# Performance work log

Hardware: AMD Instinct MI355X
Metric: run time of the kernel (lower is better)

## Reference

```python
import jax, jax.numpy as jnp
import numpy as np

WS = 8      # window size
SS = 4      # shift size
NH = 4      # num heads
EPS = 1e-5
MLP_RATIO = 4


def _win_part(x, ws):
    # x: [B,D,H,W,C] -> [B*nD*nH*nW, ws^3, C]
    B, D, H, W, C = x.shape
    x = x.reshape(B, D // ws, ws, H // ws, ws, W // ws, ws, C)
    x = x.transpose(0, 1, 3, 5, 2, 4, 6, 7)
    return x.reshape(-1, ws * ws * ws, C)


def _win_rev(w, ws, B, D, H, W):
    C = w.shape[-1]
    x = w.reshape(B, D // ws, H // ws, W // ws, ws, ws, ws, C)
    x = x.transpose(0, 1, 4, 2, 5, 3, 6, 7)
    return x.reshape(B, D, H, W, C)


def _ln(x, g, b):
    m = jnp.mean(x, axis=-1, keepdims=True)
    v = jnp.mean((x - m) ** 2, axis=-1, keepdims=True)
    return (x - m) / jnp.sqrt(v + EPS) * g + b


def _rel_index(ws):
    coords = np.stack(np.meshgrid(np.arange(ws), np.arange(ws), np.arange(ws), indexing='ij'))  # [3,ws,ws,ws]
    cf = coords.reshape(3, -1)                      # [3, ws^3]
    rel = (cf[:, :, None] - cf[:, None, :]).transpose(1, 2, 0) + (ws - 1)  # [N,N,3]
    return rel[..., 0] * (2 * ws - 1) ** 2 + rel[..., 1] * (2 * ws - 1) + rel[..., 2]


def _attn_mask(D, H, W, ws, ss):
    img = np.zeros((1, D, H, W, 1), dtype=np.float32)
    cnt = 0
    sl = (slice(0, -ws), slice(-ws, -ss), slice(-ss, None))
    for d in sl:
        for h in sl:
            for w in sl:
                img[:, d, h, w, :] = cnt
                cnt += 1
    mw = np.asarray(_win_part(jnp.asarray(img), ws))[..., 0]  # [nW, ws^3]
    diff = mw[:, None, :] - mw[:, :, None]
    return np.where(diff != 0, -100.0, 0.0).astype(np.float32)


def setup_inputs() -> dict:
    key = jax.random.key(0)
    ks = jax.random.split(key, 12)
    B, D, H, W, C = 1, 16, 64, 64, 128
    mh = MLP_RATIO * C
    s = 0.02
    return {
        'x': jax.random.normal(ks[0], (B, D, H, W, C), jnp.float32),
        'attn_mask': jnp.asarray(_attn_mask(D, H, W, WS, SS)),
        'rel_index': jnp.asarray(_rel_index(WS), jnp.int32),
        'rel_bias': jax.random.normal(ks[1], ((2 * WS - 1) ** 3, NH), jnp.float32) * s,
        'qkv_w': jax.random.normal(ks[2], (3 * C, C), jnp.float32) * s,
        'qkv_b': jnp.zeros((3 * C,), jnp.float32),
        'proj_w': jax.random.normal(ks[3], (C, C), jnp.float32) * s,
        'proj_b': jnp.zeros((C,), jnp.float32),
        'norm1_g': jnp.ones((C,), jnp.float32),
        'norm1_b': jnp.zeros((C,), jnp.float32),
        'norm2_g': jnp.ones((C,), jnp.float32),
        'norm2_b': jnp.zeros((C,), jnp.float32),
        'mlp_w1': jax.random.normal(ks[4], (mh, C), jnp.float32) * s,
        'mlp_b1': jnp.zeros((mh,), jnp.float32),
        'mlp_w2': jax.random.normal(ks[5], (C, mh), jnp.float32) * s,
        'mlp_b2': jnp.zeros((C,), jnp.float32),
    }


def reference(x, attn_mask, rel_index, rel_bias, qkv_w, qkv_b, proj_w, proj_b,
              norm1_g, norm1_b, norm2_g, norm2_b, mlp_w1, mlp_b1, mlp_w2, mlp_b2):
    B, D, H, W, C = x.shape
    ws, ss, nh = WS, SS, NH
    hd = C // nh
    scale = hd ** -0.5
    N = ws ** 3
    shortcut = x
    h = _ln(x, norm1_g, norm1_b)
    h = jnp.roll(h, (-ss, -ss, -ss), axis=(1, 2, 3))
    xw = _win_part(h, ws)                 # [B_, N, C]
    B_ = xw.shape[0]
    nW = attn_mask.shape[0]
    qkv = xw @ qkv_w.T + qkv_b            # [B_, N, 3C]
    qkv = qkv.reshape(B_, N, 3, nh, hd).transpose(2, 0, 3, 1, 4)  # [3,B_,h,N,hd]
    q, k, v = qkv[0] * scale, qkv[1], qkv[2]
    attn = jnp.einsum('bhnd,bhmd->bhnm', q, k)
    rpe = rel_bias[rel_index.reshape(-1)].reshape(N, N, nh).transpose(2, 0, 1)  # [h,N,N]
    attn = attn + rpe[None]
    attn = attn.reshape(B_ // nW, nW, nh, N, N) + attn_mask[None, :, None]
    attn = jax.nn.softmax(attn.reshape(B_, nh, N, N), axis=-1)
    out = jnp.einsum('bhnm,bhmd->bhnd', attn, v).transpose(0, 2, 1, 3).reshape(B_, N, C)
    out = out @ proj_w.T + proj_b
    out = _win_rev(out, ws, B, D, H, W)
    out = jnp.roll(out, (ss, ss, ss), axis=(1, 2, 3))
    x = shortcut + out
    h2 = _ln(x, norm2_g, norm2_b)
    h2 = jax.nn.gelu(h2 @ mlp_w1.T + mlp_b1, approximate=False)
    return x + h2 @ mlp_w2.T + mlp_b2
```

## Files before the change

### kernel.cpp

```cpp
#include <hip/hip_runtime.h>
#include <math.h>

typedef __bf16 bf16;
typedef __bf16 bf16x8 __attribute__((ext_vector_type(8)));
typedef float f32x4 __attribute__((ext_vector_type(4)));
typedef unsigned short u16;
typedef u16 u16x2 __attribute__((ext_vector_type(2)));
typedef u16 u16x4 __attribute__((ext_vector_type(4)));

__device__ __forceinline__ float b2f(u16 b) {
  return (float)__builtin_bit_cast(bf16, b);
}

__global__ void sniff_k(const unsigned* __restrict__ xw_, int* __restrict__ flag) {
  if (threadIdx.x == 0 && blockIdx.x == 0) {
    int cnt = 0;
    for (int i = 0; i < 256; i++) {
      unsigned e = (xw_[i] >> 7) & 0xFFu;
      cnt += (e >= 100u && e <= 140u) ? 1 : 0;
    }
    *flag = (cnt >= 150) ? 1 : 0;
  }
}

__global__ __launch_bounds__(256) void canon_big_k(const void* __restrict__ src,
                                                   bf16* __restrict__ dst,
                                                   const int* __restrict__ flag) {
  int i = (blockIdx.x * 256 + threadIdx.x) * 8;
  if (*flag) {
    *(bf16x8*)&dst[i] = *(const bf16x8*)((const bf16*)src + i);
  } else {
    const float* s = (const float*)src + i;
    bf16x8 v;
#pragma unroll
    for (int j = 0; j < 8; j++) v[j] = (bf16)s[j];
    *(bf16x8*)&dst[i] = v;
  }
}

struct CanonArgs {
  const void* src[13];
  bf16* dst[13];
  int n[13];
};

__global__ __launch_bounds__(256) void canon_small_k(CanonArgs a,
                                                     const int* __restrict__ flag) {
  int ti = blockIdx.y;
  int i = blockIdx.x * 256 + threadIdx.x;
  if (i >= a.n[ti]) return;
  if (*flag)
    a.dst[ti][i] = ((const bf16*)a.src[ti])[i];
  else
    a.dst[ti][i] = (bf16)((const float*)a.src[ti])[i];
}

__global__ __launch_bounds__(256) void rpe_k(const int* __restrict__ ridx,
                                             const bf16* __restrict__ rbias,
                                             bf16* __restrict__ rpeT) {
  int t = blockIdx.x * 256 + threadIdx.x;
  int q = t & 511, m = (t >> 9) & 511, h = t >> 18;
  rpeT[t] = rbias[ridx[q * 512 + m] * 4 + h];
}

template <int ROLL>
__global__ __launch_bounds__(256) void ln_k(const bf16* __restrict__ x,
                                            const bf16* __restrict__ g,
                                            const bf16* __restrict__ bsh,
                                            bf16* __restrict__ out) {
  int wave = threadIdx.x >> 6, lane = threadIdx.x & 63;
  int tok = blockIdx.x * 4 + wave;
  size_t src;
  if (ROLL) {
    int win = tok >> 9, pos = tok & 511;
    int rd = (win >> 6) * 8 + (pos >> 6);
    int rh = ((win >> 3) & 7) * 8 + ((pos >> 3) & 7);
    int rw = (win & 7) * 8 + (pos & 7);
    int od = (rd + 4) & 15, oh = (rh + 4) & 63, ow = (rw + 4) & 63;
    src = (size_t)((od * 64 + oh) * 64 + ow) * 128;
  } else {
    src = (size_t)tok * 128;
  }
  int ch = lane * 2;
  u16x2 xv = *(const u16x2*)(x + src + ch);
  float f0 = b2f(xv[0]), f1 = b2f(xv[1]);
  float s = f0 + f1, sq = f0 * f0 + f1 * f1;
#pragma unroll
  for (int d = 1; d < 64; d <<= 1) {
    s += __shfl_xor(s, d);
    sq += __shfl_xor(sq, d);
  }
  float mean = s * (1.f / 128.f);
  float var = sq * (1.f / 128.f) - mean * mean;
  float rstd = rsqrtf(fmaxf(var, 0.f) + 1e-5f);
  u16x2 gv = *(const u16x2*)(g + ch), bv = *(const u16x2*)(bsh + ch);
  u16x2 ov;
  ov[0] = __builtin_bit_cast(u16, (bf16)((f0 - mean) * rstd * b2f(gv[0]) + b2f(bv[0])));
  ov[1] = __builtin_bit_cast(u16, (bf16)((f1 - mean) * rstd * b2f(gv[1]) + b2f(bv[1])));
  *(u16x2*)(out + (size_t)tok * 128 + ch) = ov;
}

template <int EPI, int N_, int K_>
__global__ __launch_bounds__(256) void gemm_k(const bf16* __restrict__ A,
                                              const bf16* __restrict__ B,
                                              const bf16* __restrict__ bias,
                                              void* __restrict__ outv,
                                              const bf16* __restrict__ resid,
                                              const int* __restrict__ flag) {
  __shared__ __align__(16) u16 As[128 * 72];
  __shared__ __align__(16) u16 Bs[128 * 72];
  const int t = threadIdx.x;
  const int wave = t >> 6, lane = t & 63, l15 = lane & 15, quad = lane >> 4;
  const int m0 = blockIdx.x * 128, n0 = blockIdx.y * 128;
  int fl = 0;
  if constexpr (EPI == 3) fl = *flag;
  f32x4 acc[4][4] = {};
  const int wr = (wave >> 1) * 64, wc = (wave & 1) * 64;
  const int srow = t >> 3, scol = (t & 7) * 8;
  for (int kc = 0; kc < K_; kc += 64) {
    bf16x8 av[4], bv[4];
#pragma unroll
    for (int p = 0; p < 4; p++) {
      int row = p * 32 + srow;
      av[p] = *(const bf16x8*)(A + (size_t)(m0 + row) * K_ + kc + scol);
      bv[p] = *(const bf16x8*)(B + (size_t)(n0 + row) * K_ + kc + scol);
    }
    __syncthreads();
#pragma unroll
    for (int p = 0; p < 4; p++) {
      int row = p * 32 + srow;
      *(bf16x8*)&As[row * 72 + scol] = av[p];
      *(bf16x8*)&Bs[row * 72 + scol] = bv[p];
    }
    __syncthreads();
#pragma unroll
    for (int ks = 0; ks < 2; ks++) {
      bf16x8 a[4], b[4];
#pragma unroll
      for (int i = 0; i < 4; i++) {
        a[i] = *(const bf16x8*)&As[(wr + i * 16 + l15) * 72 + ks * 32 + quad * 8];
        b[i] = *(const bf16x8*)&Bs[(wc + i * 16 + l15) * 72 + ks * 32 + quad * 8];
      }
#pragma unroll
      for (int i = 0; i < 4; i++)
#pragma unroll
        for (int j = 0; j < 4; j++)
          acc[i][j] =
              __builtin_amdgcn_mfma_f32_16x16x32_bf16(a[i], b[j], acc[i][j], 0, 0, 0);
    }
  }
  const float qscale = 0.17677669529663687f;
#pragma unroll
  for (int i = 0; i < 4; i++) {
#pragma unroll
    for (int r = 0; r < 4; r++) {
      int tok = m0 + wr + i * 16 + quad * 4 + r;
      size_t obase = 0;
      if constexpr (EPI == 1) {
        int win = tok >> 9, pos = tok & 511;
        int rd = (win >> 6) * 8 + (pos >> 6);
        int rh = ((win >> 3) & 7) * 8 + ((pos >> 3) & 7);
        int rw = (win & 7) * 8 + (pos & 7);
        int od = (rd + 4) & 15, oh = (rh + 4) & 63, ow = (rw + 4) & 63;
        obase = (size_t)((od * 64 + oh) * 64 + ow) * 128;
      } else if constexpr (EPI != 0) {
        obase = (size_t)tok * N_;
      }
#pragma unroll
      for (int j = 0; j < 4; j++) {
        int gn = n0 + wc + j * 16 + l15;
        float v = acc[i][j][r] + (float)bias[gn];
        if constexpr (EPI == 0) {
          int tensor = gn >> 7, c = gn & 127, head = c >> 5, d = c & 31;
          if (tensor == 0) v *= qscale;
          int win = tok >> 9, pos = tok & 511;
          size_t off = ((((size_t)tensor * 4 + head) * 128 + win) * 512 + pos) * 32 + d;
          ((bf16*)outv)[off] = (bf16)v;
        } else if constexpr (EPI == 1) {
          v += (float)resid[obase + gn];
          ((bf16*)outv)[obase + gn] = (bf16)v;
        } else if constexpr (EPI == 2) {
          v = 0.5f * v * (1.f + erff(v * 0.70710678118654752f));
          ((bf16*)outv)[obase + gn] = (bf16)v;
        } else {
          v += (float)resid[obase + gn];
          if (fl)
            ((bf16*)outv)[obase + gn] = (bf16)v;
          else
            ((float*)outv)[obase + gn] = v;
        }
      }
    }
  }
}

__global__ __launch_bounds__(256) void attn_k(const bf16* __restrict__ qkv,
                                              const bf16* __restrict__ rpeT,
                                              bf16* __restrict__ att) {
  __shared__ __align__(16) u16 sVt[32 * 72];
  __shared__ __align__(16) u16 sP[4][32 * 72];
  __shared__ __align__(16) u16 sR[64 * 136];
  __shared__ unsigned char lbl[512];
  const int t = threadIdx.x;
  const int p = blockIdx.x;
  const int win = ((p >> 7) << 3) | (p & 7);
  const int j = (p >> 3) & 15;
  const int head = j >> 2, qc = j & 3;
  const int wave = t >> 6, lane = t & 63, l15 = lane & 15, quad = lane >> 4;

  {
    int wd = win >> 6, wh = (win >> 3) & 7, wwi = win & 7;
    for (int pp = t; pp < 512; pp += 256) {
      int gd = wd * 8 + (pp >> 6), gh = wh * 8 + ((pp >> 3) & 7),
          gw = wwi * 8 + (pp & 7);
      int ld = gd < 8 ? 0 : (gd < 12 ? 1 : 2);
      int lh = gh < 56 ? 0 : (gh < 60 ? 1 : 2);
      int lw = gw < 56 ? 0 : (gw < 60 ? 1 : 2);
      lbl[pp] = (unsigned char)((ld << 4) | (lh << 2) | lw);
    }
  }
  __syncthreads();

  const size_t hw32 = (size_t)512 * 32;
  const bf16* qp = qkv + ((size_t)(0 * 4 + head) * 128 + win) * hw32;
  const bf16* kp = qkv + ((size_t)(1 * 4 + head) * 128 + win) * hw32;
  const bf16* vp = qkv + ((size_t)(2 * 4 + head) * 128 + win) * hw32;
  const int qbase = qc * 128 + wave * 32;

  int lq[2][4];
#pragma unroll
  for (int mt = 0; mt < 2; mt++)
#pragma unroll
    for (int r = 0; r < 4; r++) lq[mt][r] = lbl[qbase + mt * 16 + quad * 4 + r];

  bf16x8 qa[2];
#pragma unroll
  for (int mt = 0; mt < 2; mt++)
    qa[mt] = *(const bf16x8*)(qp + (size_t)(qbase + mt * 16 + l15) * 32 + quad * 8);

  f32x4 O[2][2] = {};
  float ms[2][4], ls[2][4];
#pragma unroll
  for (int mt = 0; mt < 2; mt++)
#pragma unroll
    for (int r = 0; r < 4; r++) {
      ms[mt][r] = -1e30f;
      ls[mt][r] = 0.f;
    }
  const f32x4 zf = {0.f, 0.f, 0.f, 0.f};
  const bf16* rpeh = rpeT + (size_t)head * 512 * 512;

  for (int kt = 0; kt < 8; kt++) {
    __syncthreads();
    {
      int row = t >> 2, c4 = t & 3;
      bf16x8 vv = *(const bf16x8*)(vp + (size_t)(kt * 64 + row) * 32 + c4 * 8);
#pragma unroll
      for (int jj = 0; jj < 8; jj++)
        sVt[(c4 * 8 + jj) * 72 + row] = __builtin_bit_cast(u16, vv[jj]);
    }
    {
      int rr = t >> 4, cc = (t & 15) * 8;
#pragma unroll
      for (int pp = 0; pp < 4; pp++) {
        int row = pp * 16 + rr;
        bf16x8 rv = *(const bf16x8*)(rpeh + (size_t)(kt * 64 + row) * 512 +
                                     qc * 128 + cc);
        *(bf16x8*)&sR[row * 136 + cc] = rv;
      }
    }
    __syncthreads();

    f32x4 S[2][4];
#pragma unroll
    for (int nt = 0; nt < 4; nt++) {
      bf16x8 kb =
          *(const bf16x8*)(kp + (size_t)(kt * 64 + nt * 16 + l15) * 32 + quad * 8);
      S[0][nt] = __builtin_amdgcn_mfma_f32_16x16x32_bf16(qa[0], kb, zf, 0, 0, 0);
      S[1][nt] = __builtin_amdgcn_mfma_f32_16x16x32_bf16(qa[1], kb, zf, 0, 0, 0);
    }
#pragma unroll
    for (int nt = 0; nt < 4; nt++) {
      int lk = lbl[kt * 64 + nt * 16 + l15];
#pragma unroll
      for (int mt = 0; mt < 2; mt++) {
        u16x4 rv = *(const u16x4*)&sR[(nt * 16 + l15) * 136 + mt * 16 + quad * 4];
#pragma unroll
        for (int r = 0; r < 4; r++) {
          float bv = b2f(rv[r]);
          if (lq[mt][r] != lk) bv -= 100.f;
          S[mt][nt][r] += bv;
        }
      }
    }
#pragma unroll
    for (int mt = 0; mt < 2; mt++)
#pragma unroll
      for (int r = 0; r < 4; r++) {
        float mx = fmaxf(fmaxf(S[mt][0][r], S[mt][1][r]),
                         fmaxf(S[mt][2][r], S[mt][3][r]));
        mx = fmaxf(mx, __shfl_xor(mx, 1));
        mx = fmaxf(mx, __shfl_xor(mx, 2));
        mx = fmaxf(mx, __shfl_xor(mx, 4));
        mx = fmaxf(mx, __shfl_xor(mx, 8));
        float mnew = fmaxf(ms[mt][r], mx);
        float alpha = __expf(fminf(ms[mt][r] - mnew, 0.f));
        ms[mt][r] = mnew;
        float rs = 0.f;
#pragma unroll
        for (int nt = 0; nt < 4; nt++) {
          float pe = __expf(fminf(S[mt][nt][r] - mnew, 0.f));
          S[mt][nt][r] = pe;
          rs += pe;
        }
        rs += __shfl_xor(rs, 1);
        rs += __shfl_xor(rs, 2);
        rs += __shfl_xor(rs, 4);
        rs += __shfl_xor(rs, 8);
        ls[mt][r] = ls[mt][r] * alpha + rs;
        O[mt][0][r] *= alpha;
        O[mt][1][r] *= alpha;
      }
    u16* pw = sP[wave];
#pragma unroll
    for (int mt = 0; mt < 2; mt++)
#pragma unroll
      for (int nt = 0; nt < 4; nt++)
#pragma unroll
        for (int r = 0; r < 4; r++)
          pw[(mt * 16 + quad * 4 + r) * 72 + nt * 16 + l15] =
              __builtin_bit_cast(u16, (bf16)S[mt][nt][r]);
    __syncthreads();
#pragma unroll
    for (int s = 0; s < 2; s++) {
      bf16x8 pa0 = *(const bf16x8*)&pw[l15 * 72 + s * 32 + quad * 8];
      bf16x8 pa1 = *(const bf16x8*)&pw[(16 + l15) * 72 + s * 32 + quad * 8];
      bf16x8 vb0 = *(const bf16x8*)&sVt[l15 * 72 + s * 32 + quad * 8];
      bf16x8 vb1 = *(const bf16x8*)&sVt[(16 + l15) * 72 + s * 32 + quad * 8];
      O[0][0] = __builtin_amdgcn_mfma_f32_16x16x32_bf16(pa0, vb0, O[0][0], 0, 0, 0);
      O[0][1] = __builtin_amdgcn_mfma_f32_16x16x32_bf16(pa0, vb1, O[0][1], 0, 0, 0);
      O[1][0] = __builtin_amdgcn_mfma_f32_16x16x32_bf16(pa1, vb0, O[1][0], 0, 0, 0);
      O[1][1] = __builtin_amdgcn_mfma_f32_16x16x32_bf16(pa1, vb1, O[1][1], 0, 0, 0);
    }
  }
#pragma unroll
  for (int mt = 0; mt < 2; mt++)
#pragma unroll
    for (int nd = 0; nd < 2; nd++)
#pragma unroll
      for (int r = 0; r < 4; r++) {
        int q = qbase + mt * 16 + quad * 4 + r;
        att[((size_t)win * 512 + q) * 128 + head * 32 + nd * 16 + l15] =
            (bf16)(O[mt][nd][r] / ls[mt][r]);
      }
}

extern "C" void kernel_launch(void* const* d_in, const int* in_sizes, int n_in,
                              void* d_out, int out_size, void* d_ws,
                              size_t ws_size, hipStream_t stream) {
  const int* rel_index = (const int*)d_in[2];
  char* w = (char*)d_ws;

  int* flag = (int*)w;
  bf16* rb_c = (bf16*)(w + (64ull << 10));
  bf16* qw_c = (bf16*)(w + (128ull << 10));
  bf16* pw_c = (bf16*)(w + (256ull << 10));
  bf16* w1_c = (bf16*)(w + (320ull << 10));
  bf16* w2_c = (bf16*)(w + (512ull << 10));
  bf16* qb_c = (bf16*)(w + (704ull << 10));
  bf16* pb_c = (bf16*)(w + (708ull << 10));
  bf16* g1_c = (bf16*)(w + (712ull << 10));
  bf16* b1n_c = (bf16*)(w + (716ull << 10));
  bf16* g2_c = (bf16*)(w + (720ull << 10));
  bf16* b2n_c = (bf16*)(w + (724ull << 10));
  bf16* mb1_c = (bf16*)(w + (728ull << 10));
  bf16* mb2_c = (bf16*)(w + (732ull << 10));
  bf16* x_c = (bf16*)(w + (1ull << 20));
  bf16* xw = (bf16*)(w + (17ull << 20));
  bf16* qkvb = (bf16*)(w + (33ull << 20));
  bf16* rpeT = (bf16*)(w + (97ull << 20));
  bf16* x2 = (bf16*)(w + (99ull << 20));
  bf16* att = xw;
  bf16* h2 = xw;
  bf16* a1 = qkvb;

  sniff_k<<<1, 64, 0, stream>>>((const unsigned*)d_in[0], flag);
  canon_big_k<<<4096, 256, 0, stream>>>(d_in[0], x_c, flag);

  CanonArgs ca;
  const int srcidx[13] = {3, 4, 5, 6, 7, 8, 9, 10, 11, 12, 13, 14, 15};
  bf16* dsts[13] = {rb_c, qw_c, qb_c, pw_c, pb_c, g1_c, b1n_c,
                    g2_c, b2n_c, w1_c, mb1_c, w2_c, mb2_c};
  for (int i = 0; i < 13; i++) {
    ca.src[i] = d_in[srcidx[i]];
    ca.dst[i] = dsts[i];
    ca.n[i] = in_sizes[srcidx[i]];
  }
  canon_small_k<<<dim3(256, 13), 256, 0, stream>>>(ca, flag);

  rpe_k<<<4096, 256, 0, stream>>>(rel_index, rb_c, rpeT);
  ln_k<1><<<16384, 256, 0, stream>>>(x_c, g1_c, b1n_c, xw);
  gemm_k<0, 384, 128><<<dim3(512, 3), 256, 0, stream>>>(xw, qw_c, qb_c, qkvb,
                                                        nullptr, flag);
  attn_k<<<2048, 256, 0, stream>>>(qkvb, rpeT, att);
  gemm_k<1, 128, 128><<<dim3(512, 1), 256, 0, stream>>>(att, pw_c, pb_c, x2,
                                                        x_c, flag);
  ln_k<0><<<16384, 256, 0, stream>>>(x2, g2_c, b2n_c, h2);
  gemm_k<2, 512, 128><<<dim3(512, 4), 256, 0, stream>>>(h2, w1_c, mb1_c, a1,
                                                        nullptr, flag);
  gemm_k<3, 128, 512><<<dim3(512, 1), 256, 0, stream>>>(a1, w2_c, mb2_c, d_out,
                                                        x2, flag);
}
```

Baseline: 454.2 us.

## Transpose attention MFMA orientation and load bias directly into accumulator

Swaps the QK^T MFMA operands so each lane owns a query column, which turns the softmax row reductions into two cross-quad shuffles instead of four. The relative-position bias is stored untransposed, read straight from global memory and fed in as the MFMA accumulator init. This removes the shared-memory bias staging and one barrier per key tile. The shift mask labels are computed and compared only for windows that touch the shifted boundary. The output is written as vector bf16x4 stores using a reciprocal, and the flag sniff becomes a wave-parallel reduction; the direct global bias reads may be less coalesced than the old staged copy.

```diff
diff --git a/kernel.cpp b/kernel.cpp
--- a/kernel.cpp
+++ b/kernel.cpp
@@ -2,25 +2,27 @@
 #include <math.h>
 
 typedef __bf16 bf16;
+typedef __bf16 bf16x4 __attribute__((ext_vector_type(4)));
 typedef __bf16 bf16x8 __attribute__((ext_vector_type(8)));
 typedef float f32x4 __attribute__((ext_vector_type(4)));
 typedef unsigned short u16;
 typedef u16 u16x2 __attribute__((ext_vector_type(2)));
-typedef u16 u16x4 __attribute__((ext_vector_type(4)));
 
 __device__ __forceinline__ float b2f(u16 b) {
   return (float)__builtin_bit_cast(bf16, b);
 }
 
 __global__ void sniff_k(const unsigned* __restrict__ xw_, int* __restrict__ flag) {
-  if (threadIdx.x == 0 && blockIdx.x == 0) {
-    int cnt = 0;
-    for (int i = 0; i < 256; i++) {
-      unsigned e = (xw_[i] >> 7) & 0xFFu;
-      cnt += (e >= 100u && e <= 140u) ? 1 : 0;
-    }
-    *flag = (cnt >= 150) ? 1 : 0;
-  }
+  int lane = threadIdx.x;
+  int c = 0;
+#pragma unroll
+  for (int j = 0; j < 4; j++) {
+    unsigned e = (xw_[lane * 4 + j] >> 7) & 0xFFu;
+    c += (e >= 100u && e <= 140u) ? 1 : 0;
+  }
+#pragma unroll
+  for (int d = 1; d < 64; d <<= 1) c += __shfl_xor(c, d);
+  if (lane == 0) *flag = (c >= 150) ? 1 : 0;
 }
 
 __global__ __launch_bounds__(256) void canon_big_k(const void* __restrict__ src,
@@ -57,10 +59,10 @@
 
 __global__ __launch_bounds__(256) void rpe_k(const int* __restrict__ ridx,
                                              const bf16* __restrict__ rbias,
-                                             bf16* __restrict__ rpeT) {
+                                             bf16* __restrict__ rpe) {
   int t = blockIdx.x * 256 + threadIdx.x;
-  int q = t & 511, m = (t >> 9) & 511, h = t >> 18;
-  rpeT[t] = rbias[ridx[q * 512 + m] * 4 + h];
+  int m = t & 511, q = (t >> 9) & 511, h = t >> 18;
+  rpe[t] = rbias[ridx[q * 512 + m] * 4 + h];
 }
 
 template <int ROLL>
@@ -195,12 +197,11 @@
 }
 
 __global__ __launch_bounds__(256) void attn_k(const bf16* __restrict__ qkv,
-                                              const bf16* __restrict__ rpeT,
+                                              const bf16* __restrict__ rpe,
                                               bf16* __restrict__ att) {
-  __shared__ __align__(16) u16 sVt[32 * 72];
-  __shared__ __align__(16) u16 sP[4][32 * 72];
-  __shared__ __align__(16) u16 sR[64 * 136];
-  __shared__ unsigned char lbl[512];
+  __shared__ __align__(16) bf16 sVt[32 * 72];
+  __shared__ __align__(16) bf16 sP[4][32 * 72];
+  __shared__ __align__(4) unsigned char lbl[512];
   const int t = threadIdx.x;
   const int p = blockIdx.x;
   const int win = ((p >> 7) << 3) | (p & 7);
@@ -208,11 +209,12 @@
   const int head = j >> 2, qc = j & 3;
   const int wave = t >> 6, lane = t & 63, l15 = lane & 15, quad = lane >> 4;
 
-  {
-    int wd = win >> 6, wh = (win >> 3) & 7, wwi = win & 7;
+  const int wd = win >> 6, wh = (win >> 3) & 7, ww = win & 7;
+  const bool wm = (wd == 1) || (wh == 7) || (ww == 7);
+  if (wm) {
     for (int pp = t; pp < 512; pp += 256) {
       int gd = wd * 8 + (pp >> 6), gh = wh * 8 + ((pp >> 3) & 7),
-          gw = wwi * 8 + (pp & 7);
+          gw = ww * 8 + (pp & 7);
       int ld = gd < 8 ? 0 : (gd < 12 ? 1 : 2);
       int lh = gh < 56 ? 0 : (gh < 60 ? 1 : 2);
       int lw = gw < 56 ? 0 : (gw < 60 ? 1 : 2);
@@ -225,30 +227,28 @@
   const bf16* qp = qkv + ((size_t)(0 * 4 + head) * 128 + win) * hw32;
   const bf16* kp = qkv + ((size_t)(1 * 4 + head) * 128 + win) * hw32;
   const bf16* vp = qkv + ((size_t)(2 * 4 + head) * 128 + win) * hw32;
+  const bf16* rpeh = rpe + (size_t)head * 512 * 512;
   const int qbase = qc * 128 + wave * 32;
 
-  int lq[2][4];
-#pragma unroll
-  for (int mt = 0; mt < 2; mt++)
-#pragma unroll
-    for (int r = 0; r < 4; r++) lq[mt][r] = lbl[qbase + mt * 16 + quad * 4 + r];
+  int lq[2] = {0, 0};
+  if (wm) {
+#pragma unroll
+    for (int nt = 0; nt < 2; nt++) lq[nt] = lbl[qbase + nt * 16 + l15];
+  }
 
   bf16x8 qa[2];
 #pragma unroll
-  for (int mt = 0; mt < 2; mt++)
-    qa[mt] = *(const bf16x8*)(qp + (size_t)(qbase + mt * 16 + l15) * 32 + quad * 8);
+  for (int nt = 0; nt < 2; nt++)
+    qa[nt] = *(const bf16x8*)(qp + (size_t)(qbase + nt * 16 + l15) * 32 + quad * 8);
 
   f32x4 O[2][2] = {};
-  float ms[2][4], ls[2][4];
-#pragma unroll
-  for (int mt = 0; mt < 2; mt++)
-#pragma unroll
-    for (int r = 0; r < 4; r++) {
-      ms[mt][r] = -1e30f;
-      ls[mt][r] = 0.f;
-    }
-  const f32x4 zf = {0.f, 0.f, 0.f, 0.f};
-  const bf16* rpeh = rpeT + (size_t)head * 512 * 512;
+  float ms[2], ls[2];
+#pragma unroll
+  for (int nt = 0; nt < 2; nt++) {
+    ms[nt] = -1e30f;
+    ls[nt] = 0.f;
+  }
+  bf16* pw = sP[wave];
 
   for (int kt = 0; kt < 8; kt++) {
     __syncthreads();
@@ -256,103 +256,92 @@
       int row = t >> 2, c4 = t & 3;
       bf16x8 vv = *(const bf16x8*)(vp + (size_t)(kt * 64 + row) * 32 + c4 * 8);
 #pragma unroll
-      for (int jj = 0; jj < 8; jj++)
-        sVt[(c4 * 8 + jj) * 72 + row] = __builtin_bit_cast(u16, vv[jj]);
-    }
-    {
-      int rr = t >> 4, cc = (t & 15) * 8;
-#pragma unroll
-      for (int pp = 0; pp < 4; pp++) {
-        int row = pp * 16 + rr;
-        bf16x8 rv = *(const bf16x8*)(rpeh + (size_t)(kt * 64 + row) * 512 +
-                                     qc * 128 + cc);
-        *(bf16x8*)&sR[row * 136 + cc] = rv;
+      for (int jj = 0; jj < 8; jj++) sVt[(c4 * 8 + jj) * 72 + row] = vv[jj];
+    }
+    __syncthreads();
+
+    f32x4 S[4][2];
+#pragma unroll
+    for (int mt = 0; mt < 4; mt++) {
+      bf16x8 kb =
+          *(const bf16x8*)(kp + (size_t)(kt * 64 + mt * 16 + l15) * 32 + quad * 8);
+      int kcb = kt * 64 + mt * 16 + quad * 4;
+      unsigned kl4 = 0;
+      if (wm) kl4 = *(const unsigned*)&lbl[kcb];
+#pragma unroll
+      for (int nt = 0; nt < 2; nt++) {
+        bf16x4 rv = *(const bf16x4*)(rpeh + (size_t)(qbase + nt * 16 + l15) * 512 + kcb);
+        f32x4 c;
+#pragma unroll
+        for (int r = 0; r < 4; r++) {
+          float bv = (float)rv[r];
+          if (wm && (int)((kl4 >> (8 * r)) & 0xFF) != lq[nt]) bv -= 100.f;
+          c[r] = bv;
+        }
+        S[mt][nt] = __builtin_amdgcn_mfma_f32_16x16x32_bf16(kb, qa[nt], c, 0, 0, 0);
       }
     }
-    __syncthreads();
-
-    f32x4 S[2][4];
-#pragma unroll
-    for (int nt = 0; nt < 4; nt++) {
-      bf16x8 kb =
-          *(const bf16x8*)(kp + (size_t)(kt * 64 + nt * 16 + l15) * 32 + quad * 8);
-      S[0][nt] = __builtin_amdgcn_mfma_f32_16x16x32_bf16(qa[0], kb, zf, 0, 0, 0);
-      S[1][nt] = __builtin_amdgcn_mfma_f32_16x16x32_bf16(qa[1], kb, zf, 0, 0, 0);
-    }
-#pragma unroll
-    for (int nt = 0; nt < 4; nt++) {
-      int lk = lbl[kt * 64 + nt * 16 + l15];
-#pragma unroll
-      for (int mt = 0; mt < 2; mt++) {
-        u16x4 rv = *(const u16x4*)&sR[(nt * 16 + l15) * 136 + mt * 16 + quad * 4];
+#pragma unroll
+    for (int nt = 0; nt < 2; nt++) {
+      float mx = -1e30f;
+#pragma unroll
+      for (int mt = 0; mt < 4; mt++)
+#pragma unroll
+        for (int r = 0; r < 4; r++) mx = fmaxf(mx, S[mt][nt][r]);
+      mx = fmaxf(mx, __shfl_xor(mx, 16));
+      mx = fmaxf(mx, __shfl_xor(mx, 32));
+      float mnew = fmaxf(ms[nt], mx);
+      float alpha = __expf(ms[nt] - mnew);
+      ms[nt] = mnew;
+      float rs = 0.f;
+#pragma unroll
+      for (int mt = 0; mt < 4; mt++)
 #pragma unroll
         for (int r = 0; r < 4; r++) {
-          float bv = b2f(rv[r]);
-          if (lq[mt][r] != lk) bv -= 100.f;
-          S[mt][nt][r] += bv;
-        }
-      }
-    }
-#pragma unroll
-    for (int mt = 0; mt < 2; mt++)
-#pragma unroll
-      for (int r = 0; r < 4; r++) {
-        float mx = fmaxf(fmaxf(S[mt][0][r], S[mt][1][r]),
-                         fmaxf(S[mt][2][r], S[mt][3][r]));
-        mx = fmaxf(mx, __shfl_xor(mx, 1));
-        mx = fmaxf(mx, __shfl_xor(mx, 2));
-        mx = fmaxf(mx, __shfl_xor(mx, 4));
-        mx = fmaxf(mx, __shfl_xor(mx, 8));
-        float mnew = fmaxf(ms[mt][r], mx);
-        float alpha = __expf(fminf(ms[mt][r] - mnew, 0.f));
-        ms[mt][r] = mnew;
-        float rs = 0.f;
-#pragma unroll
-        for (int nt = 0; nt < 4; nt++) {
-          float pe = __expf(fminf(S[mt][nt][r] - mnew, 0.f));
+          float pe = __expf(S[mt][nt][r] - mnew);
           S[mt][nt][r] = pe;
           rs += pe;
         }
-        rs += __shfl_xor(rs, 1);
-        rs += __shfl_xor(rs, 2);
-        rs += __shfl_xor(rs, 4);
-        rs += __shfl_xor(rs, 8);
-        ls[mt][r] = ls[mt][r] * alpha + rs;
-        O[mt][0][r] *= alpha;
-        O[mt][1][r] *= alpha;
+      rs += __shfl_xor(rs, 16);
+      rs += __shfl_xor(rs, 32);
+      ls[nt] = ls[nt] * alpha + rs;
+      O[0][nt] *= alpha;
+      O[1][nt] *= alpha;
+    }
+#pragma unroll
+    for (int nt = 0; nt < 2; nt++)
+#pragma unroll
+      for (int mt = 0; mt < 4; mt++) {
+        bf16x4 pv;
+#pragma unroll
+        for (int r = 0; r < 4; r++) pv[r] = (bf16)S[mt][nt][r];
+        *(bf16x4*)&pw[(nt * 16 + l15) * 72 + mt * 16 + quad * 4] = pv;
       }
-    u16* pw = sP[wave];
-#pragma unroll
-    for (int mt = 0; mt < 2; mt++)
-#pragma unroll
-      for (int nt = 0; nt < 4; nt++)
-#pragma unroll
-        for (int r = 0; r < 4; r++)
-          pw[(mt * 16 + quad * 4 + r) * 72 + nt * 16 + l15] =
-              __builtin_bit_cast(u16, (bf16)S[mt][nt][r]);
-    __syncthreads();
 #pragma unroll
     for (int s = 0; s < 2; s++) {
-      bf16x8 pa0 = *(const bf16x8*)&pw[l15 * 72 + s * 32 + quad * 8];
-      bf16x8 pa1 = *(const bf16x8*)&pw[(16 + l15) * 72 + s * 32 + quad * 8];
-      bf16x8 vb0 = *(const bf16x8*)&sVt[l15 * 72 + s * 32 + quad * 8];
-      bf16x8 vb1 = *(const bf16x8*)&sVt[(16 + l15) * 72 + s * 32 + quad * 8];
-      O[0][0] = __builtin_amdgcn_mfma_f32_16x16x32_bf16(pa0, vb0, O[0][0], 0, 0, 0);
-      O[0][1] = __builtin_amdgcn_mfma_f32_16x16x32_bf16(pa0, vb1, O[0][1], 0, 0, 0);
-      O[1][0] = __builtin_amdgcn_mfma_f32_16x16x32_bf16(pa1, vb0, O[1][0], 0, 0, 0);
-      O[1][1] = __builtin_amdgcn_mfma_f32_16x16x32_bf16(pa1, vb1, O[1][1], 0, 0, 0);
-    }
-  }
-#pragma unroll
-  for (int mt = 0; mt < 2; mt++)
-#pragma unroll
-    for (int nd = 0; nd < 2; nd++)
-#pragma unroll
-      for (int r = 0; r < 4; r++) {
-        int q = qbase + mt * 16 + quad * 4 + r;
-        att[((size_t)win * 512 + q) * 128 + head * 32 + nd * 16 + l15] =
-            (bf16)(O[mt][nd][r] / ls[mt][r]);
-      }
+      bf16x8 va0 = *(const bf16x8*)&sVt[l15 * 72 + s * 32 + quad * 8];
+      bf16x8 va1 = *(const bf16x8*)&sVt[(16 + l15) * 72 + s * 32 + quad * 8];
+      bf16x8 pb0 = *(const bf16x8*)&pw[l15 * 72 + s * 32 + quad * 8];
+      bf16x8 pb1 = *(const bf16x8*)&pw[(16 + l15) * 72 + s * 32 + quad * 8];
+      O[0][0] = __builtin_amdgcn_mfma_f32_16x16x32_bf16(va0, pb0, O[0][0], 0, 0, 0);
+      O[0][1] = __builtin_amdgcn_mfma_f32_16x16x32_bf16(va0, pb1, O[0][1], 0, 0, 0);
+      O[1][0] = __builtin_amdgcn_mfma_f32_16x16x32_bf16(va1, pb0, O[1][0], 0, 0, 0);
+      O[1][1] = __builtin_amdgcn_mfma_f32_16x16x32_bf16(va1, pb1, O[1][1], 0, 0, 0);
+    }
+  }
+#pragma unroll
+  for (int nt = 0; nt < 2; nt++) {
+    float inv = __builtin_amdgcn_rcpf(ls[nt]);
+    int q = qbase + nt * 16 + l15;
+#pragma unroll
+    for (int dm = 0; dm < 2; dm++) {
+      bf16x4 o;
+#pragma unroll
+      for (int r = 0; r < 4; r++) o[r] = (bf16)(O[dm][nt][r] * inv);
+      *(bf16x4*)(att + ((size_t)win * 512 + q) * 128 + head * 32 + dm * 16 +
+                 quad * 4) = o;
+    }
+  }
 }
 
 extern "C" void kernel_launch(void* const* d_in, const int* in_sizes, int n_in,
@@ -378,7 +367,7 @@
   bf16* x_c = (bf16*)(w + (1ull << 20));
   bf16* xw = (bf16*)(w + (17ull << 20));
   bf16* qkvb = (bf16*)(w + (33ull << 20));
-  bf16* rpeT = (bf16*)(w + (97ull << 20));
+  bf16* rpe = (bf16*)(w + (97ull << 20));
   bf16* x2 = (bf16*)(w + (99ull << 20));
   bf16* att = xw;
   bf16* h2 = xw;
@@ -398,11 +387,11 @@
   }
   canon_small_k<<<dim3(256, 13), 256, 0, stream>>>(ca, flag);
 
-  rpe_k<<<4096, 256, 0, stream>>>(rel_index, rb_c, rpeT);
+  rpe_k<<<4096, 256, 0, stream>>>(rel_index, rb_c, rpe);
   ln_k<1><<<16384, 256, 0, stream>>>(x_c, g1_c, b1n_c, xw);
   gemm_k<0, 384, 128><<<dim3(512, 3), 256, 0, stream>>>(xw, qw_c, qb_c, qkvb,
                                                         nullptr, flag);
-  attn_k<<<2048, 256, 0, stream>>>(qkvb, rpeT, att);
+  attn_k<<<2048, 256, 0, stream>>>(qkvb, rpe, att);
   gemm_k<1, 128, 128><<<dim3(512, 1), 256, 0, stream>>>(att, pw_c, pb_c, x2,
                                                         x_c, flag);
   ln_k<0><<<16384, 256, 0, stream>>>(x2, g2_c, b2n_c, h2);
```

Measured after the change: 439.5 us. 3.2% less time.
